# Optimization experiments

Measured on AMD Instinct MI355X. Metric: run time of the kernel, lower is better.

## Reference

```python
import jax, jax.numpy as jnp
import numpy as np

IN_F = 4096
OUT_F = 4096
BATCH = 4096


def _dequantize(q, mn, mx):
    # Faithful to dequantize_to_float32: per-tensor affine using the *observed*
    # integer min/max of the stored tensor.
    q_min = q.min()
    q_max = q.max()
    scale = (mx - mn) / (q_max - q_min).astype(jnp.float32)
    return (q - q_min).astype(jnp.float32) * scale + mn


def setup_inputs() -> dict:
    key = jax.random.key(0)
    k1, k2, k3 = jax.random.split(key, 3)
    x = jax.random.normal(k1, (BATCH, IN_F), dtype=jnp.float32)
    # int8-valued weights/bias stored as int32 (same math; dequant uses tensor min/max)
    weight_q = jax.random.randint(k2, (OUT_F, IN_F), -128, 128, dtype=jnp.int32)
    bias_q = jax.random.randint(k3, (OUT_F,), -128, 128, dtype=jnp.int32)
    # per-tensor float range recorded at quantization time (original scales by 255 first,
    # so these ranges are on the scaled tensor; any floats work for correctness testing)
    weight_min = jnp.float32(-4.2)
    weight_max = jnp.float32(4.5)
    bias_min = jnp.float32(-1.3)
    bias_max = jnp.float32(1.1)
    return {
        "x": x,
        "weight_q": weight_q,
        "bias_q": bias_q,
        "weight_min": weight_min,
        "weight_max": weight_max,
        "bias_min": bias_min,
        "bias_max": bias_max,
    }


def reference(x, weight_q, bias_q, weight_min, weight_max, bias_min, bias_max):
    w = _dequantize(weight_q, weight_min, weight_max)   # [OUT_F, IN_F] fp32
    b = _dequantize(bias_q, bias_min, bias_max)         # [OUT_F] fp32
    # F.linear: x @ W^T + b
    return jnp.einsum("bi,oi->bo", x, w) + b
```

## Files before the change

kernel.cpp:

```cpp
#include <hip/hip_runtime.h>
#include <climits>

#define IN_F 4096
#define OUT_F 4096
#define BATCH 4096
#define NPART 1024

typedef __bf16 bf16x8 __attribute__((ext_vector_type(8)));
typedef float f32x4 __attribute__((ext_vector_type(4)));

__device__ __forceinline__ unsigned short f2bf_rne(float f) {
  unsigned int u = __float_as_uint(f);
  u += 0x7fffu + ((u >> 16) & 1u);
  return (unsigned short)(u >> 16);
}

__global__ __launch_bounds__(256) void k_conv(const float* __restrict__ x,
                                              const int* __restrict__ q,
                                              unsigned short* __restrict__ xb,
                                              unsigned short* __restrict__ qb,
                                              float* __restrict__ rowsum,
                                              int* __restrict__ pmin,
                                              int* __restrict__ pmax) {
  if (blockIdx.x < NPART) {
    const int n4 = (OUT_F * IN_F) / 4;
    const int stride = NPART * 256;
    int vmin = INT_MAX, vmax = INT_MIN;
    const int4* q4 = (const int4*)q;
    ushort4* qb4 = (ushort4*)qb;
    for (int i = blockIdx.x * 256 + threadIdx.x; i < n4; i += stride) {
      int4 v = q4[i];
      vmin = min(vmin, min(min(v.x, v.y), min(v.z, v.w)));
      vmax = max(vmax, max(max(v.x, v.y), max(v.z, v.w)));
      ushort4 h;
      h.x = f2bf_rne((float)v.x);
      h.y = f2bf_rne((float)v.y);
      h.z = f2bf_rne((float)v.z);
      h.w = f2bf_rne((float)v.w);
      qb4[i] = h;
    }
    for (int off = 32; off > 0; off >>= 1) {
      vmin = min(vmin, __shfl_down(vmin, off));
      vmax = max(vmax, __shfl_down(vmax, off));
    }
    __shared__ int rmin[4], rmax[4];
    const int wave = threadIdx.x >> 6;
    if ((threadIdx.x & 63) == 0) { rmin[wave] = vmin; rmax[wave] = vmax; }
    __syncthreads();
    if (threadIdx.x == 0) {
      pmin[blockIdx.x] = min(min(rmin[0], rmin[1]), min(rmin[2], rmin[3]));
      pmax[blockIdx.x] = max(max(rmax[0], rmax[1]), max(rmax[2], rmax[3]));
    }
  } else {
    const int wave = threadIdx.x >> 6;
    const int lane = threadIdx.x & 63;
    const int row = (blockIdx.x - NPART) * 4 + wave;
    const float4* xr = (const float4*)(x + (size_t)row * IN_F);
    ushort4* xbr = (ushort4*)(xb + (size_t)row * IN_F);
    float s = 0.f;
#pragma unroll
    for (int it = 0; it < IN_F / 4 / 64; ++it) {
      const int i = it * 64 + lane;
      float4 v = xr[i];
      s += (v.x + v.y) + (v.z + v.w);
      ushort4 h;
      h.x = f2bf_rne(v.x); h.y = f2bf_rne(v.y);
      h.z = f2bf_rne(v.z); h.w = f2bf_rne(v.w);
      xbr[i] = h;
    }
    for (int off = 32; off > 0; off >>= 1) s += __shfl_down(s, off);
    if (lane == 0) rowsum[row] = s;
  }
}

__global__ __launch_bounds__(256) void k_wmm(const int* __restrict__ q,
                                             int* __restrict__ pmin,
                                             int* __restrict__ pmax) {
  const int n4 = (OUT_F * IN_F) / 4;
  const int stride = gridDim.x * blockDim.x;
  int vmin = INT_MAX, vmax = INT_MIN;
  const int4* q4 = (const int4*)q;
  for (int i = blockIdx.x * blockDim.x + threadIdx.x; i < n4; i += stride) {
    int4 v = q4[i];
    vmin = min(vmin, min(min(v.x, v.y), min(v.z, v.w)));
    vmax = max(vmax, max(max(v.x, v.y), max(v.z, v.w)));
  }
  for (int off = 32; off > 0; off >>= 1) {
    vmin = min(vmin, __shfl_down(vmin, off));
    vmax = max(vmax, __shfl_down(vmax, off));
  }
  __shared__ int rmin[4], rmax[4];
  const int wave = threadIdx.x >> 6;
  if ((threadIdx.x & 63) == 0) { rmin[wave] = vmin; rmax[wave] = vmax; }
  __syncthreads();
  if (threadIdx.x == 0) {
    pmin[blockIdx.x] = min(min(rmin[0], rmin[1]), min(rmin[2], rmin[3]));
    pmax[blockIdx.x] = max(max(rmax[0], rmax[1]), max(rmax[2], rmax[3]));
  }
}

__global__ __launch_bounds__(256) void k_scal(const int* __restrict__ pmin,
                                              const int* __restrict__ pmax, int npart,
                                              const int* __restrict__ bq,
                                              const float* __restrict__ wmn,
                                              const float* __restrict__ wmx,
                                              const float* __restrict__ bmn,
                                              const float* __restrict__ bmx,
                                              float* __restrict__ scal) {
  int vmin = INT_MAX, vmax = INT_MIN;
  for (int i = threadIdx.x; i < npart; i += 256) {
    vmin = min(vmin, pmin[i]);
    vmax = max(vmax, pmax[i]);
  }
  int bmin = INT_MAX, bmaxv = INT_MIN;
  for (int i = threadIdx.x; i < OUT_F; i += 256) {
    int v = bq[i];
    bmin = min(bmin, v);
    bmaxv = max(bmaxv, v);
  }
  for (int off = 32; off > 0; off >>= 1) {
    vmin = min(vmin, __shfl_down(vmin, off));
    vmax = max(vmax, __shfl_down(vmax, off));
    bmin = min(bmin, __shfl_down(bmin, off));
    bmaxv = max(bmaxv, __shfl_down(bmaxv, off));
  }
  __shared__ int r[4][4];
  const int wave = threadIdx.x >> 6;
  if ((threadIdx.x & 63) == 0) {
    r[wave][0] = vmin; r[wave][1] = vmax; r[wave][2] = bmin; r[wave][3] = bmaxv;
  }
  __syncthreads();
  if (threadIdx.x == 0) {
    int qmin = min(min(r[0][0], r[1][0]), min(r[2][0], r[3][0]));
    int qmax = max(max(r[0][1], r[1][1]), max(r[2][1], r[3][1]));
    int qbmin = min(min(r[0][2], r[1][2]), min(r[2][2], r[3][2]));
    int qbmax = max(max(r[0][3], r[1][3]), max(r[2][3], r[3][3]));
    float ws = (*wmx - *wmn) / (float)(qmax - qmin);
    scal[0] = ws;
    scal[1] = *wmn - ws * (float)qmin;
    float bs = (*bmx - *bmn) / (float)(qbmax - qbmin);
    scal[2] = bs;
    scal[3] = *bmn - bs * (float)qbmin;
  }
}

__device__ __forceinline__ void load_lds16(const unsigned short* g, unsigned short* l) {
  __builtin_amdgcn_global_load_lds(
      (const __attribute__((address_space(1))) unsigned int*)g,
      (__attribute__((address_space(3))) unsigned int*)l, 16, 0, 0);
}

#define VMW(n) asm volatile("s_waitcnt vmcnt(" #n ")" ::: "memory")
#define CFENCE asm volatile("" ::: "memory")

#define GITER(C, CA, CB, NA, NB, PF, LDN, CHK)                                      \
  {                                                                                 \
    bf16x8 a2_[4];                                                                  \
    _Pragma("unroll") for (int i = 0; i < 4; ++i)                                   \
        a2_[i] = *(const bf16x8*)&As[(C)][(wm + 64 + i * 16 + r16) * 32 + pc];      \
    if (PF) {                                                                       \
      load_lds16(srcA0 + kb + ((C) + 3) * 32, &As[((C) + 3) & 3][dst0]);            \
      load_lds16(srcA1 + kb + ((C) + 3) * 32, &As[((C) + 3) & 3][dst1]);            \
    }                                                                               \
    __builtin_amdgcn_s_setprio(1);                                                  \
    _Pragma("unroll") for (int mi = 0; mi < 4; ++mi)                                \
        _Pragma("unroll") for (int ni = 0; ni < 4; ++ni)                            \
            acc[mi][ni] = __builtin_amdgcn_mfma_f32_16x16x32_bf16(                  \
                CA[mi], CB[ni], acc[mi][ni], 0, 0, 0);                              \
    __builtin_amdgcn_s_setprio(0);                                                  \
    if (LDN) {                                                                      \
      _Pragma("unroll") for (int i = 0; i < 4; ++i) {                               \
        NA[i] = *(const bf16x8*)&As[((C) + 1) & 3][(wm + i * 16 + r16) * 32 + pc];  \
        NB[i] = *(const bf16x8*)&Bs[((C) + 1) & 3][(wn + i * 16 + r16) * 32 + pc];  \
      }                                                                             \
    }                                                                               \
    if (PF) {                                                                       \
      load_lds16(srcB0 + kb + ((C) + 3) * 32, &Bs[((C) + 3) & 3][dst0]);            \
      load_lds16(srcB1 + kb + ((C) + 3) * 32, &Bs[((C) + 3) & 3][dst1]);            \
    }                                                                               \
    __builtin_amdgcn_s_setprio(1);                                                  \
    _Pragma("unroll") for (int mi = 0; mi < 4; ++mi)                                \
        _Pragma("unroll") for (int ni = 0; ni < 4; ++ni)                            \
            acc[4 + mi][ni] = __builtin_amdgcn_mfma_f32_16x16x32_bf16(              \
                a2_[mi], CB[ni], acc[4 + mi][ni], 0, 0, 0);                         \
    __builtin_amdgcn_s_setprio(0);                                                  \
    CHK;                                                                            \
    __builtin_amdgcn_s_barrier();                                                   \
    CFENCE;                                                                         \
  }

__global__ __launch_bounds__(512, 2) void k_gemm(
    const unsigned short* __restrict__ A,
    const unsigned short* __restrict__ B,
    const int* __restrict__ bq,
    const float* __restrict__ rowsum,
    const float* __restrict__ scal,
    float* __restrict__ C) {
  __shared__ __align__(16) unsigned short As[4][8192];
  __shared__ __align__(16) unsigned short Bs[4][8192];

  const int tid = threadIdx.x;
  const int w = tid >> 6;
  const int lane = tid & 63;
  const int bm = blockIdx.x * 256;
  const int bn = blockIdx.y * 256;

  const int wm = (w & 1) * 128;
  const int wn = (w >> 1) * 64;
  const int r16 = lane & 15;
  const int q = lane >> 4;
  const int pc = (q ^ ((r16 >> 1) & 3)) * 8;

  const int cA0 = w * 128 + lane;
  const int rowS0 = cA0 >> 2;
  const int colS0 = ((cA0 & 3) ^ ((rowS0 >> 1) & 3)) * 8;
  const int cA1 = cA0 + 64;
  const int rowS1 = cA1 >> 2;
  const int colS1 = ((cA1 & 3) ^ ((rowS1 >> 1) & 3)) * 8;
  const unsigned short* srcA0 = A + (size_t)(bm + rowS0) * IN_F + colS0;
  const unsigned short* srcA1 = A + (size_t)(bm + rowS1) * IN_F + colS1;
  const unsigned short* srcB0 = B + (size_t)(bn + rowS0) * IN_F + colS0;
  const unsigned short* srcB1 = B + (size_t)(bn + rowS1) * IN_F + colS1;
  const int dst0 = w * 1024;
  const int dst1 = w * 1024 + 512;

  f32x4 acc[8][4] = {};
  bf16x8 fa0[4], fb0[4], fa1[4], fb1[4];

#pragma unroll
  for (int t = 0; t < 3; ++t) {
    load_lds16(srcA0 + t * 32, &As[t][dst0]);
    load_lds16(srcA1 + t * 32, &As[t][dst1]);
    load_lds16(srcB0 + t * 32, &Bs[t][dst0]);
    load_lds16(srcB1 + t * 32, &Bs[t][dst1]);
  }
  VMW(4);
  __builtin_amdgcn_s_barrier();
  CFENCE;
#pragma unroll
  for (int i = 0; i < 4; ++i) {
    fa0[i] = *(const bf16x8*)&As[0][(wm + i * 16 + r16) * 32 + pc];
    fb0[i] = *(const bf16x8*)&Bs[0][(wn + i * 16 + r16) * 32 + pc];
  }

  for (int u = 0; u < 31; ++u) {
    const int kb = u * 128;
    GITER(0, fa0, fb0, fa1, fb1, 1, 1, VMW(4));
    GITER(1, fa1, fb1, fa0, fb0, 1, 1, VMW(4));
    GITER(2, fa0, fb0, fa1, fb1, 1, 1, VMW(4));
    GITER(3, fa1, fb1, fa0, fb0, 1, 1, VMW(4));
  }
  {
    const int kb = 31 * 128;
    GITER(0, fa0, fb0, fa1, fb1, 1, 1, VMW(4));
    GITER(1, fa1, fb1, fa0, fb0, 0, 1, VMW(0));
    GITER(2, fa0, fb0, fa1, fb1, 0, 1, ((void)0));
    GITER(3, fa1, fb1, fa0, fb0, 0, 0, ((void)0));
  }

  const float wsc = scal[0], wbe = scal[1], bsc = scal[2], bbe = scal[3];
#pragma unroll
  for (int ni = 0; ni < 4; ++ni) {
    const int gn = bn + wn + ni * 16 + r16;
    const float bdq = bsc * (float)bq[gn] + bbe;
#pragma unroll
    for (int mi = 0; mi < 8; ++mi) {
      const int gm0 = bm + wm + mi * 16 + q * 4;
#pragma unroll
      for (int r = 0; r < 4; ++r) {
        const int gm = gm0 + r;
        C[(size_t)gm * OUT_F + gn] = wsc * acc[mi][ni][r] + wbe * rowsum[gm] + bdq;
      }
    }
  }
}

__global__ void k_naive(const float* __restrict__ x, const int* __restrict__ wq,
                        const int* __restrict__ bq, const float* __restrict__ scal,
                        float* __restrict__ out) {
  const int o = blockIdx.x * blockDim.x + threadIdx.x;
  const int b = blockIdx.y;
  const float* xr = x + (size_t)b * IN_F;
  const int* wr = wq + (size_t)o * IN_F;
  float s = 0.f, sx = 0.f;
  for (int k = 0; k < IN_F; ++k) {
    float xv = xr[k];
    s += xv * (float)wr[k];
    sx += xv;
  }
  out[(size_t)b * OUT_F + o] =
      scal[0] * s + scal[1] * sx + scal[2] * (float)bq[o] + scal[3];
}

extern "C" void kernel_launch(void* const* d_in, const int* in_sizes, int n_in,
                              void* d_out, int out_size, void* d_ws, size_t ws_size,
                              hipStream_t stream) {
  const float* x = (const float*)d_in[0];
  const int* wq = (const int*)d_in[1];
  const int* bq = (const int*)d_in[2];
  const float* wmn = (const float*)d_in[3];
  const float* wmx = (const float*)d_in[4];
  const float* bmn = (const float*)d_in[5];
  const float* bmx = (const float*)d_in[6];
  float* out = (float*)d_out;

  char* ws = (char*)d_ws;
  float* scal = (float*)ws;
  int* pmin = (int*)(ws + 64);
  int* pmax = (int*)(ws + 64 + NPART * 4);
  float* rowsum = (float*)(ws + 64 + 2 * NPART * 4);
  unsigned short* xb = (unsigned short*)(ws + 32768);
  unsigned short* qb = xb + (size_t)BATCH * IN_F;
  const size_t needed = 32768 + (size_t)BATCH * IN_F * 2 + (size_t)OUT_F * IN_F * 2;

  if (ws_size >= needed) {
    k_conv<<<2 * NPART, 256, 0, stream>>>(x, wq, xb, qb, rowsum, pmin, pmax);
    k_scal<<<1, 256, 0, stream>>>(pmin, pmax, NPART, bq, wmn, wmx, bmn, bmx, scal);
    dim3 grid(BATCH / 256, OUT_F / 256);
    k_gemm<<<grid, 512, 0, stream>>>(xb, qb, bq, rowsum, scal, out);
  } else {
    k_wmm<<<NPART, 256, 0, stream>>>(wq, pmin, pmax);
    k_scal<<<1, 256, 0, stream>>>(pmin, pmax, NPART, bq, wmn, wmx, bmn, bmx, scal);
    k_naive<<<dim3(OUT_F / 256, BATCH), 256, 0, stream>>>(x, wq, bq, scal, out);
  }
}
```

Before: 314.4 us.

## Split conversion kernel, widen to 8-element stores, fold scale computation into GEMM

The single conversion kernel is split into separate weight and activation kernels, and each thread now loads two 16-byte vectors and writes one 16-byte bf16 vector. The separate single-block k_scal launch is removed. Every GEMM block now reduces the 1024 partial min/max values and the bias min/max itself, computing the dequant scales in LDS. This drops one launch and a serial tiny kernel, but every GEMM block repeats the reduction, and the split adds a launch between the two conversion passes.

Result: no change. 316.7 us (+0.7%).

```diff
diff --git a/kernel.cpp b/kernel.cpp
--- a/kernel.cpp
+++ b/kernel.cpp
@@ -8,6 +8,7 @@
 
 typedef __bf16 bf16x8 __attribute__((ext_vector_type(8)));
 typedef float f32x4 __attribute__((ext_vector_type(4)));
+typedef unsigned short u16x8 __attribute__((ext_vector_type(8)));
 
 __device__ __forceinline__ unsigned short f2bf_rne(float f) {
   unsigned int u = __float_as_uint(f);
@@ -15,62 +16,67 @@
   return (unsigned short)(u >> 16);
 }
 
-__global__ __launch_bounds__(256) void k_conv(const float* __restrict__ x,
-                                              const int* __restrict__ q,
-                                              unsigned short* __restrict__ xb,
-                                              unsigned short* __restrict__ qb,
-                                              float* __restrict__ rowsum,
-                                              int* __restrict__ pmin,
-                                              int* __restrict__ pmax) {
-  if (blockIdx.x < NPART) {
-    const int n4 = (OUT_F * IN_F) / 4;
-    const int stride = NPART * 256;
-    int vmin = INT_MAX, vmax = INT_MIN;
-    const int4* q4 = (const int4*)q;
-    ushort4* qb4 = (ushort4*)qb;
-    for (int i = blockIdx.x * 256 + threadIdx.x; i < n4; i += stride) {
-      int4 v = q4[i];
-      vmin = min(vmin, min(min(v.x, v.y), min(v.z, v.w)));
-      vmax = max(vmax, max(max(v.x, v.y), max(v.z, v.w)));
-      ushort4 h;
-      h.x = f2bf_rne((float)v.x);
-      h.y = f2bf_rne((float)v.y);
-      h.z = f2bf_rne((float)v.z);
-      h.w = f2bf_rne((float)v.w);
-      qb4[i] = h;
-    }
-    for (int off = 32; off > 0; off >>= 1) {
-      vmin = min(vmin, __shfl_down(vmin, off));
-      vmax = max(vmax, __shfl_down(vmax, off));
-    }
-    __shared__ int rmin[4], rmax[4];
-    const int wave = threadIdx.x >> 6;
-    if ((threadIdx.x & 63) == 0) { rmin[wave] = vmin; rmax[wave] = vmax; }
-    __syncthreads();
-    if (threadIdx.x == 0) {
-      pmin[blockIdx.x] = min(min(rmin[0], rmin[1]), min(rmin[2], rmin[3]));
-      pmax[blockIdx.x] = max(max(rmax[0], rmax[1]), max(rmax[2], rmax[3]));
-    }
-  } else {
-    const int wave = threadIdx.x >> 6;
-    const int lane = threadIdx.x & 63;
-    const int row = (blockIdx.x - NPART) * 4 + wave;
-    const float4* xr = (const float4*)(x + (size_t)row * IN_F);
-    ushort4* xbr = (ushort4*)(xb + (size_t)row * IN_F);
-    float s = 0.f;
-#pragma unroll
-    for (int it = 0; it < IN_F / 4 / 64; ++it) {
-      const int i = it * 64 + lane;
-      float4 v = xr[i];
-      s += (v.x + v.y) + (v.z + v.w);
-      ushort4 h;
-      h.x = f2bf_rne(v.x); h.y = f2bf_rne(v.y);
-      h.z = f2bf_rne(v.z); h.w = f2bf_rne(v.w);
-      xbr[i] = h;
-    }
-    for (int off = 32; off > 0; off >>= 1) s += __shfl_down(s, off);
-    if (lane == 0) rowsum[row] = s;
-  }
+__global__ __launch_bounds__(256) void k_convW(const int* __restrict__ q,
+                                               unsigned short* __restrict__ qb,
+                                               int* __restrict__ pmin,
+                                               int* __restrict__ pmax) {
+  const int n8 = (OUT_F * IN_F) / 8;
+  const int stride = NPART * 256;
+  int vmin = INT_MAX, vmax = INT_MIN;
+  const int4* q4 = (const int4*)q;
+  u16x8* qb8 = (u16x8*)qb;
+  for (int i = blockIdx.x * 256 + threadIdx.x; i < n8; i += stride) {
+    int4 a = q4[2 * i];
+    int4 b = q4[2 * i + 1];
+    vmin = min(vmin, min(min(min(a.x, a.y), min(a.z, a.w)),
+                         min(min(b.x, b.y), min(b.z, b.w))));
+    vmax = max(vmax, max(max(max(a.x, a.y), max(a.z, a.w)),
+                         max(max(b.x, b.y), max(b.z, b.w))));
+    u16x8 h;
+    h[0] = f2bf_rne((float)a.x); h[1] = f2bf_rne((float)a.y);
+    h[2] = f2bf_rne((float)a.z); h[3] = f2bf_rne((float)a.w);
+    h[4] = f2bf_rne((float)b.x); h[5] = f2bf_rne((float)b.y);
+    h[6] = f2bf_rne((float)b.z); h[7] = f2bf_rne((float)b.w);
+    qb8[i] = h;
+  }
+  for (int off = 32; off > 0; off >>= 1) {
+    vmin = min(vmin, __shfl_down(vmin, off));
+    vmax = max(vmax, __shfl_down(vmax, off));
+  }
+  __shared__ int rmin[4], rmax[4];
+  const int wave = threadIdx.x >> 6;
+  if ((threadIdx.x & 63) == 0) { rmin[wave] = vmin; rmax[wave] = vmax; }
+  __syncthreads();
+  if (threadIdx.x == 0) {
+    pmin[blockIdx.x] = min(min(rmin[0], rmin[1]), min(rmin[2], rmin[3]));
+    pmax[blockIdx.x] = max(max(rmax[0], rmax[1]), max(rmax[2], rmax[3]));
+  }
+}
+
+__global__ __launch_bounds__(256) void k_convX(const float* __restrict__ x,
+                                               unsigned short* __restrict__ xb,
+                                               float* __restrict__ rowsum) {
+  const int wave = threadIdx.x >> 6;
+  const int lane = threadIdx.x & 63;
+  const int row = blockIdx.x * 4 + wave;
+  const float4* xr = (const float4*)(x + (size_t)row * IN_F);
+  u16x8* xbr = (u16x8*)(xb + (size_t)row * IN_F);
+  float s = 0.f;
+#pragma unroll
+  for (int it = 0; it < IN_F / 8 / 64; ++it) {
+    const int i = it * 64 + lane;
+    float4 v0 = xr[2 * i];
+    float4 v1 = xr[2 * i + 1];
+    s += ((v0.x + v0.y) + (v0.z + v0.w)) + ((v1.x + v1.y) + (v1.z + v1.w));
+    u16x8 h;
+    h[0] = f2bf_rne(v0.x); h[1] = f2bf_rne(v0.y);
+    h[2] = f2bf_rne(v0.z); h[3] = f2bf_rne(v0.w);
+    h[4] = f2bf_rne(v1.x); h[5] = f2bf_rne(v1.y);
+    h[6] = f2bf_rne(v1.z); h[7] = f2bf_rne(v1.w);
+    xbr[i] = h;
+  }
+  for (int off = 32; off > 0; off >>= 1) s += __shfl_down(s, off);
+  if (lane == 0) rowsum[row] = s;
 }
 
 __global__ __launch_bounds__(256) void k_wmm(const int* __restrict__ q,
@@ -194,16 +200,56 @@
     const unsigned short* __restrict__ B,
     const int* __restrict__ bq,
     const float* __restrict__ rowsum,
-    const float* __restrict__ scal,
+    const int* __restrict__ pmin,
+    const int* __restrict__ pmax,
+    const float* __restrict__ wmn, const float* __restrict__ wmx,
+    const float* __restrict__ bmn, const float* __restrict__ bmx,
     float* __restrict__ C) {
   __shared__ __align__(16) unsigned short As[4][8192];
   __shared__ __align__(16) unsigned short Bs[4][8192];
+  __shared__ int rr[8][4];
+  __shared__ float s_scal[4];
 
   const int tid = threadIdx.x;
   const int w = tid >> 6;
   const int lane = tid & 63;
   const int bm = blockIdx.x * 256;
   const int bn = blockIdx.y * 256;
+
+  {
+    int vmin = INT_MAX, vmax = INT_MIN;
+    for (int i = tid; i < NPART; i += 512) {
+      vmin = min(vmin, pmin[i]);
+      vmax = max(vmax, pmax[i]);
+    }
+    int bmn_ = INT_MAX, bmx_ = INT_MIN;
+    for (int i = tid; i < OUT_F; i += 512) {
+      int v = bq[i];
+      bmn_ = min(bmn_, v);
+      bmx_ = max(bmx_, v);
+    }
+    for (int off = 32; off > 0; off >>= 1) {
+      vmin = min(vmin, __shfl_down(vmin, off));
+      vmax = max(vmax, __shfl_down(vmax, off));
+      bmn_ = min(bmn_, __shfl_down(bmn_, off));
+      bmx_ = max(bmx_, __shfl_down(bmx_, off));
+    }
+    if ((tid & 63) == 0) { rr[w][0] = vmin; rr[w][1] = vmax; rr[w][2] = bmn_; rr[w][3] = bmx_; }
+    __syncthreads();
+    if (tid == 0) {
+      int qmin = rr[0][0], qmax = rr[0][1], qbmin = rr[0][2], qbmax = rr[0][3];
+      for (int i = 1; i < 8; ++i) {
+        qmin = min(qmin, rr[i][0]); qmax = max(qmax, rr[i][1]);
+        qbmin = min(qbmin, rr[i][2]); qbmax = max(qbmax, rr[i][3]);
+      }
+      float ws = (*wmx - *wmn) / (float)(qmax - qmin);
+      s_scal[0] = ws;
+      s_scal[1] = *wmn - ws * (float)qmin;
+      float bs = (*bmx - *bmn) / (float)(qbmax - qbmin);
+      s_scal[2] = bs;
+      s_scal[3] = *bmn - bs * (float)qbmin;
+    }
+  }
 
   const int wm = (w & 1) * 128;
   const int wn = (w >> 1) * 64;
@@ -258,7 +304,7 @@
     GITER(3, fa1, fb1, fa0, fb0, 0, 0, ((void)0));
   }
 
-  const float wsc = scal[0], wbe = scal[1], bsc = scal[2], bbe = scal[3];
+  const float wsc = s_scal[0], wbe = s_scal[1], bsc = s_scal[2], bbe = s_scal[3];
 #pragma unroll
   for (int ni = 0; ni < 4; ++ni) {
     const int gn = bn + wn + ni * 16 + r16;
@@ -314,10 +360,11 @@
   const size_t needed = 32768 + (size_t)BATCH * IN_F * 2 + (size_t)OUT_F * IN_F * 2;
 
   if (ws_size >= needed) {
-    k_conv<<<2 * NPART, 256, 0, stream>>>(x, wq, xb, qb, rowsum, pmin, pmax);
-    k_scal<<<1, 256, 0, stream>>>(pmin, pmax, NPART, bq, wmn, wmx, bmn, bmx, scal);
+    k_convW<<<NPART, 256, 0, stream>>>(wq, qb, pmin, pmax);
+    k_convX<<<BATCH / 4, 256, 0, stream>>>(x, xb, rowsum);
     dim3 grid(BATCH / 256, OUT_F / 256);
-    k_gemm<<<grid, 512, 0, stream>>>(xb, qb, bq, rowsum, scal, out);
+    k_gemm<<<grid, 512, 0, stream>>>(xb, qb, bq, rowsum, pmin, pmax,
+                                     wmn, wmx, bmn, bmx, out);
   } else {
     k_wmm<<<NPART, 256, 0, stream>>>(wq, pmin, pmax);
     k_scal<<<1, 256, 0, stream>>>(pmin, pmax, NPART, bq, wmn, wmx, bmn, bmx, scal);
```
